# Optimization experiments

Measured on AMD Instinct MI355X. Metric: run time of the kernel, lower is better.

The kernel has to match this reference:

```python
import jax, jax.numpy as jnp
import numpy as np

B, S, H, L = 64, 512, 768, 21


def setup_inputs() -> dict:
    key = jax.random.key(0)
    ks = jax.random.split(key, 8)
    hidden = jax.random.normal(ks[0], (B, S, H), dtype=jnp.float32)
    attention_mask = jnp.ones((B, S), dtype=jnp.int32)
    labels = jax.random.randint(ks[1], (B, S), 0, L, dtype=jnp.int64)
    W = jax.random.normal(ks[2], (H, L), dtype=jnp.float32) * 0.02
    b = jnp.zeros((L,), dtype=jnp.float32)
    start_transitions = jax.random.uniform(ks[3], (L,), minval=-0.1, maxval=0.1)
    end_transitions = jax.random.uniform(ks[4], (L,), minval=-0.1, maxval=0.1)
    transitions = jax.random.uniform(ks[5], (L, L), minval=-0.1, maxval=0.1)
    return {"hidden": hidden, "attention_mask": attention_mask, "labels": labels,
            "W": W, "b": b, "start_transitions": start_transitions,
            "end_transitions": end_transitions, "transitions": transitions}


def _crf_llh(emissions, tags, mask, start, end, trans):
    # torchcrf log-likelihood, batch_first. emissions [B,S,L], tags [B,S], mask [B,S] bool
    maskf = mask.astype(emissions.dtype)
    first_tags = tags[:, 0]
    num = start[first_tags] + jnp.take_along_axis(emissions[:, 0], first_tags[:, None], axis=1)[:, 0]
    trans_scores = trans[tags[:, :-1], tags[:, 1:]]                         # [B,S-1]
    emit_scores = jnp.take_along_axis(emissions, tags[:, :, None], axis=2)[:, :, 0]  # [B,S]
    num = num + jnp.sum((trans_scores + emit_scores[:, 1:]) * maskf[:, 1:], axis=1)
    seq_ends = jnp.sum(mask.astype(jnp.int32), axis=1) - 1
    last_tags = jnp.take_along_axis(tags, seq_ends[:, None], axis=1)[:, 0]
    num = num + end[last_tags]
    # denominator: forward algorithm as a scan over time
    def step(score, xs):
        emit_t, m_t = xs  # [B,L], [B]
        nxt = jax.nn.logsumexp(score[:, :, None] + trans[None] + emit_t[:, None, :], axis=1)
        return jnp.where(m_t[:, None], nxt, score), None
    score0 = start[None] + emissions[:, 0]
    xs = (jnp.transpose(emissions[:, 1:], (1, 0, 2)), mask[:, 1:].T)
    scoreT, _ = jax.lax.scan(step, score0, xs)
    denom = jax.nn.logsumexp(scoreT + end[None], axis=1)
    return num - denom


def _viterbi_one_hot(emissions, mask, start, end, trans):
    # Viterbi decode (max-plus scan) + backtrack, returns one-hot logits like _decoded_to_one_hot
    def fstep(score, xs):
        emit_t, m_t = xs
        cand = score[:, :, None] + trans[None]     # [B,L,L]
        idx = jnp.argmax(cand, axis=1)             # [B,L] best previous tag
        nxt = jnp.max(cand, axis=1) + emit_t
        return jnp.where(m_t[:, None], nxt, score), idx
    score0 = start[None] + emissions[:, 0]
    xs = (jnp.transpose(emissions[:, 1:], (1, 0, 2)), mask[:, 1:].T)
    scoreT, hist = jax.lax.scan(fstep, score0, xs)   # hist [S-1,B,L]
    best_last = jnp.argmax(scoreT + end[None], axis=1)  # [B]
    def bstep(carry, xs):
        h_t, m_t = xs
        prev = jnp.take_along_axis(h_t, carry[:, None], axis=1)[:, 0]
        return jnp.where(m_t, prev, carry), carry
    tag0, tags_rest = jax.lax.scan(bstep, best_last, (hist, mask[:, 1:].T), reverse=True)
    tags = jnp.concatenate([tag0[:, None], tags_rest.T], axis=1)  # [B,S]
    one_hot = jax.nn.one_hot(tags, emissions.shape[-1], dtype=emissions.dtype)
    return one_hot * mask[:, :, None].astype(emissions.dtype)


def reference(hidden, attention_mask, labels, W, b, start_transitions, end_transitions, transitions):
    mask = attention_mask.astype(bool)
    emissions = jnp.einsum('bsh,hl->bsl', hidden, W) + b  # classifier (dropout = identity in eval)
    logits = _viterbi_one_hot(emissions, mask, start_transitions, end_transitions, transitions)
    # loss path: replicate forward's tag/mask fixups
    tags = jnp.where(labels < 0, 0, labels).at[:, 0].set(0)
    valid = (mask & (labels >= 0)).at[:, 0].set(True)
    llh = _crf_llh(emissions, tags, valid, start_transitions, end_transitions, transitions)
    loss = -jnp.mean(llh)
    return loss, logits
```

## Files before the change

kernel.cpp:

```cpp
#include <hip/hip_runtime.h>
#include <math.h>

#define BB 64
#define SS 512
#define HH 768
#define LL 21
#define STR 513
#define INFF __builtin_huge_valf()

__device__ inline float rlf(float v, int i) {
    return __int_as_float(__builtin_amdgcn_readlane(__float_as_int(v), i));
}
__device__ inline float mx3(float a, float b, float c) { return fmaxf(fmaxf(a, b), c); }
__device__ inline float wmax64(float v) {
    #pragma unroll
    for (int off = 32; off; off >>= 1) v = fmaxf(v, __shfl_xor(v, off));
    return v;
}
__device__ inline float rlmax21(float a) {
    float r0 = mx3(rlf(a, 0), rlf(a, 1), rlf(a, 2));
    float r1 = mx3(rlf(a, 3), rlf(a, 4), rlf(a, 5));
    float r2 = mx3(rlf(a, 6), rlf(a, 7), rlf(a, 8));
    float r3 = mx3(rlf(a, 9), rlf(a, 10), rlf(a, 11));
    float r4 = mx3(rlf(a, 12), rlf(a, 13), rlf(a, 14));
    float r5 = mx3(rlf(a, 15), rlf(a, 16), rlf(a, 17));
    float r6 = mx3(rlf(a, 18), rlf(a, 19), rlf(a, 20));
    return mx3(mx3(r0, r1, r2), mx3(r3, r4, r5), r6);
}

__global__ __launch_bounds__(128) void k_emis(const float* __restrict__ hidden,
                                              const float* __restrict__ W,
                                              const float* __restrict__ bias,
                                              float* __restrict__ em0,
                                              float* __restrict__ em1,
                                              float* __restrict__ em2,
                                              float* __restrict__ em3) {
    __shared__ float Wl[192 * 24];
    int tid = threadIdx.x;
    int q = blockIdx.x & 3;
    int rg = blockIdx.x >> 2;
    int row = rg * 128 + tid;
    const float* hp = hidden + (size_t)row * HH + q * 192;
    const float4* Wq4 = reinterpret_cast<const float4*>(W + q * 192 * LL);

    for (int f = tid; f < 1008; f += 128) {
        float4 v = Wq4[f];
        int e0 = 4 * f;
        { int e = e0,     k = e / 21, l = e - 21 * k; Wl[k * 24 + l] = v.x; }
        { int e = e0 + 1, k = e / 21, l = e - 21 * k; Wl[k * 24 + l] = v.y; }
        { int e = e0 + 2, k = e / 21, l = e - 21 * k; Wl[k * 24 + l] = v.z; }
        { int e = e0 + 3, k = e / 21, l = e - 21 * k; Wl[k * 24 + l] = v.w; }
    }
    __syncthreads();

    float acc[LL];
    #pragma unroll
    for (int l = 0; l < LL; ++l) acc[l] = 0.f;

#define FMAK(HV, WB) do { \
    float hv_ = (HV); \
    float4 q0 = *reinterpret_cast<const float4*>(WB); \
    float4 q1 = *reinterpret_cast<const float4*>((WB) + 4); \
    float4 q2 = *reinterpret_cast<const float4*>((WB) + 8); \
    float4 q3 = *reinterpret_cast<const float4*>((WB) + 12); \
    float4 q4 = *reinterpret_cast<const float4*>((WB) + 16); \
    float q20 = (WB)[20]; \
    acc[0]  = fmaf(hv_, q0.x, acc[0]);  acc[1]  = fmaf(hv_, q0.y, acc[1]); \
    acc[2]  = fmaf(hv_, q0.z, acc[2]);  acc[3]  = fmaf(hv_, q0.w, acc[3]); \
    acc[4]  = fmaf(hv_, q1.x, acc[4]);  acc[5]  = fmaf(hv_, q1.y, acc[5]); \
    acc[6]  = fmaf(hv_, q1.z, acc[6]);  acc[7]  = fmaf(hv_, q1.w, acc[7]); \
    acc[8]  = fmaf(hv_, q2.x, acc[8]);  acc[9]  = fmaf(hv_, q2.y, acc[9]); \
    acc[10] = fmaf(hv_, q2.z, acc[10]); acc[11] = fmaf(hv_, q2.w, acc[11]); \
    acc[12] = fmaf(hv_, q3.x, acc[12]); acc[13] = fmaf(hv_, q3.y, acc[13]); \
    acc[14] = fmaf(hv_, q3.z, acc[14]); acc[15] = fmaf(hv_, q3.w, acc[15]); \
    acc[16] = fmaf(hv_, q4.x, acc[16]); acc[17] = fmaf(hv_, q4.y, acc[17]); \
    acc[18] = fmaf(hv_, q4.z, acc[18]); acc[19] = fmaf(hv_, q4.w, acc[19]); \
    acc[20] = fmaf(hv_, q20, acc[20]); } while (0)

    float4 ha = *reinterpret_cast<const float4*>(hp);
    for (int c = 0; c < 48; ++c) {
        float4 hn = ha;
        if (c + 1 < 48) hn = *reinterpret_cast<const float4*>(hp + (c + 1) * 4);
        const float* wb = Wl + (c * 4) * 24;
        FMAK(ha.x, wb);
        FMAK(ha.y, wb + 24);
        FMAK(ha.z, wb + 48);
        FMAK(ha.w, wb + 72);
        ha = hn;
    }
#undef FMAK

    float* emr = (q == 0 ? em0 : q == 1 ? em1 : q == 2 ? em2 : em3) + (size_t)row * LL;
    if (q == 0) {
        #pragma unroll
        for (int l = 0; l < LL; ++l) emr[l] = acc[l] + bias[l];
    } else {
        #pragma unroll
        for (int l = 0; l < LL; ++l) emr[l] = acc[l];
    }
}

__global__ __launch_bounds__(64) void k_scan(const float* __restrict__ em0,
                                             const float* __restrict__ em1,
                                             const float* __restrict__ em2,
                                             const float* __restrict__ em3,
                                             const int* __restrict__ attn,
                                             const int* __restrict__ labels,
                                             const float* __restrict__ startT,
                                             const float* __restrict__ endT,
                                             const float* __restrict__ trans,
                                             float* __restrict__ num,
                                             float* __restrict__ denom,
                                             float* __restrict__ Sout) {
    __shared__ float eLT[LL * STR + 8];
    int lane = threadIdx.x;
    int bid = blockIdx.x;
    bool act = lane < LL;
    int jj = act ? lane : (LL - 1);

    if (bid < 128) {
        int b = bid & 63;
        size_t boff = (size_t)b * SS * LL;
        const float* emb0 = em0 + boff;
        const float* emb1 = em1 + boff;
        const float* emb2 = em2 + boff;
        const float* emb3 = em3 + boff;
        const int* mrow = attn + b * SS;

        for (int f = lane; f < (SS * LL) / 4; f += 64) {
            float4 v0 = *reinterpret_cast<const float4*>(emb0 + 4 * f);
            float4 v1 = *reinterpret_cast<const float4*>(emb1 + 4 * f);
            float4 v2 = *reinterpret_cast<const float4*>(emb2 + 4 * f);
            float4 v3 = *reinterpret_cast<const float4*>(emb3 + 4 * f);
            float4 v = make_float4((v0.x + v1.x) + (v2.x + v3.x),
                                   (v0.y + v1.y) + (v2.y + v3.y),
                                   (v0.z + v1.z) + (v2.z + v3.z),
                                   (v0.w + v1.w) + (v2.w + v3.w));
            unsigned e0 = 4u * (unsigned)f;
            { unsigned t = e0 / 21u,       j = e0 - 21u * t;       eLT[j * STR + t] = v.x; }
            { unsigned e = e0 + 1, t = e / 21u, j = e - 21u * t;   eLT[j * STR + t] = v.y; }
            { unsigned e = e0 + 2, t = e / 21u, j = e - 21u * t;   eLT[j * STR + t] = v.z; }
            { unsigned e = e0 + 3, t = e / 21u, j = e - 21u * t;   eLT[j * STR + t] = v.w; }
        }
        __syncthreads();

        int jbase = jj * STR;
        float A0, A1, A2, A3, B0, B1, B2, B3;

#define LDG(P, G) do { int t4_ = (G) * 4; \
    P##0 = eLT[jbase + t4_];     P##1 = eLT[jbase + t4_ + 1]; \
    P##2 = eLT[jbase + t4_ + 2]; P##3 = eLT[jbase + t4_ + 3]; } while (0)

        if (bid < 64) {
            float Tc[LL];
            #pragma unroll
            for (int i = 0; i < LL; ++i) Tc[i] = trans[i * LL + jj];
            float* Sgj = Sout + (size_t)b * (LL * SS) + jj * SS;

#define VCORE(EMIT, BIT) do { \
    float sv_[LL]; \
    _Pragma("unroll") for (int i_ = 0; i_ < LL; ++i_) sv_[i_] = rlf(a, i_); \
    __builtin_amdgcn_sched_barrier(0); \
    float cd_[LL]; \
    _Pragma("unroll") for (int i_ = 0; i_ < LL; ++i_) cd_[i_] = sv_[i_] + Tc[i_]; \
    float x0 = mx3(cd_[0], cd_[1], cd_[2]),   x1 = mx3(cd_[3], cd_[4], cd_[5]); \
    float x2 = mx3(cd_[6], cd_[7], cd_[8]),   x3 = mx3(cd_[9], cd_[10], cd_[11]); \
    float x4 = mx3(cd_[12], cd_[13], cd_[14]), x5 = mx3(cd_[15], cd_[16], cd_[17]); \
    float x6 = mx3(cd_[18], cd_[19], cd_[20]); \
    float best = mx3(mx3(x0, x1, x2), mx3(x3, x4, x5), x6); \
    bool mt_ = ((mm >> (BIT)) & 1ull) != 0ull; \
    float an_ = best + (EMIT); \
    a = (mt_ && act) ? an_ : a; \
} while (0)
#define VGROUPR(P, TB, BB0) do { \
    float o0_, o1_, o2_, o3_; \
    VCORE(P##0, (BB0));     o0_ = a; \
    VCORE(P##1, (BB0) + 1); o1_ = a; \
    VCORE(P##2, (BB0) + 2); o2_ = a; \
    VCORE(P##3, (BB0) + 3); o3_ = a; \
    if (act) *reinterpret_cast<float4*>(Sgj + (TB)) = make_float4(o0_, o1_, o2_, o3_); \
} while (0)

            LDG(A, 0); LDG(B, 1);
            int mk0 = mrow[lane];
            unsigned long long mm = __ballot(mk0 != 0);
            mk0 = mrow[64 + lane];
            float a = act ? (startT[lane] + A0) : -INFF;
            {
                float o0_ = a, o1_, o2_, o3_;
                VCORE(A1, 1); o1_ = a;
                VCORE(A2, 2); o2_ = a;
                VCORE(A3, 3); o3_ = a;
                if (act) *reinterpret_cast<float4*>(Sgj) = make_float4(o0_, o1_, o2_, o3_);
                LDG(A, 2);
                VGROUPR(B, 4, 4);
                LDG(B, 3);
            }
            for (int gg = 1; gg < 64; ++gg) {
                if ((gg & 7) == 0) {
                    mm = __ballot(mk0 != 0);
                    if (gg != 56) mk0 = mrow[((gg >> 3) + 1) * 64 + lane];
                }
                int bb = (gg & 7) * 8;
                VGROUPR(A, 8 * gg, bb);
                LDG(A, 2 * gg + 2);
                VGROUPR(B, 8 * gg + 4, bb + 4);
                LDG(B, 2 * gg + 3);
            }
#undef VCORE
#undef VGROUPR
        } else {
            float Ec[LL];
            #pragma unroll
            for (int i = 0; i < LL; ++i) Ec[i] = __expf(trans[i * LL + jj]);

#define LCORE(EMIT, BIT) do { \
    float x_ = __expf(a - M); \
    float sv_[LL]; \
    _Pragma("unroll") for (int i_ = 0; i_ < LL; ++i_) sv_[i_] = rlf(x_, i_); \
    __builtin_amdgcn_sched_barrier(0); \
    float g0_ = sv_[0] * Ec[0]; \
    _Pragma("unroll") for (int i_ = 1; i_ < 7; ++i_)  g0_ = fmaf(sv_[i_], Ec[i_], g0_); \
    float g1_ = sv_[7] * Ec[7]; \
    _Pragma("unroll") for (int i_ = 8; i_ < 14; ++i_) g1_ = fmaf(sv_[i_], Ec[i_], g1_); \
    float g2_ = sv_[14] * Ec[14]; \
    _Pragma("unroll") for (int i_ = 15; i_ < 21; ++i_) g2_ = fmaf(sv_[i_], Ec[i_], g2_); \
    float Ss_ = (g0_ + g1_) + g2_; \
    bool mt_ = ((mm >> (BIT)) & 1ull) != 0ull; \
    float an_ = M + __logf(Ss_) + (EMIT); \
    a = (mt_ && act) ? an_ : a; \
} while (0)

            LDG(A, 0); LDG(B, 1);
            int mk0 = mrow[lane];
            unsigned long long mm = __ballot(mk0 != 0);
            mk0 = mrow[64 + lane];
            float a = act ? (startT[lane] + A0) : -INFF;
            float M = rlmax21(a);
            {
                LCORE(A1, 1); LCORE(A2, 2); LCORE(A3, 3);
                LDG(A, 2);
                LCORE(B0, 4); LCORE(B1, 5); LCORE(B2, 6); LCORE(B3, 7);
                LDG(B, 3);
            }
            for (int gg = 1; gg < 64; ++gg) {
                if ((gg & 7) == 0) {
                    mm = __ballot(mk0 != 0);
                    if (gg != 56) mk0 = mrow[((gg >> 3) + 1) * 64 + lane];
                }
                M = rlmax21(a);
                int bb = (gg & 7) * 8;
                LCORE(A0, bb);     LCORE(A1, bb + 1); LCORE(A2, bb + 2); LCORE(A3, bb + 3);
                LDG(A, 2 * gg + 2);
                LCORE(B0, bb + 4); LCORE(B1, bb + 5); LCORE(B2, bb + 6); LCORE(B3, bb + 7);
                LDG(B, 2 * gg + 3);
            }
#undef LCORE
            float f = act ? (a + endT[lane]) : -INFF;
            float m = wmax64(f);
            float p = act ? __expf(f - m) : 0.f;
            #pragma unroll
            for (int off = 32; off; off >>= 1) p += __shfl_xor(p, off);
            if (lane == 0) denom[b] = m + __logf(p);
        }
#undef LDG
    } else {
        int b = bid - 128;
        const int* lrow = labels + b * SS;
        const int* arow = attn + b * SS;
        float psum = 0.f;
        int pcnt = 0;
        for (int s = 0; s < 8; ++s) {
            int t = s * 64 + lane;
            int lab = lrow[t];
            int mk = arow[t];
            int valid = (t == 0) ? 1 : ((mk != 0 && lab >= 0) ? 1 : 0);
            if (t >= 1 && valid) {
                int tag = (lab < 0) ? 0 : lab;
                int labp = lrow[t - 1];
                int tagp = (t == 1) ? 0 : ((labp < 0) ? 0 : labp);
                size_t ei = ((size_t)b * SS + t) * LL + tag;
                psum += trans[tagp * LL + tag] + ((em0[ei] + em1[ei]) + (em2[ei] + em3[ei]));
            }
            pcnt += valid;
        }
        #pragma unroll
        for (int off = 32; off; off >>= 1) {
            psum += __shfl_xor(psum, off);
            pcnt += __shfl_xor(pcnt, off);
        }
        int ts = pcnt - 1;
        int labL = lrow[ts];
        int tagL = (ts == 0) ? 0 : ((labL < 0) ? 0 : labL);
        if (lane == 0) {
            size_t e0i = (size_t)b * SS * LL;
            num[b] = startT[0] + ((em0[e0i] + em1[e0i]) + (em2[e0i] + em3[e0i]))
                   + psum + endT[tagL];
        }
    }
}

__global__ __launch_bounds__(512) void k_back(const float* __restrict__ S,
                                              const int* __restrict__ attn,
                                              const float* __restrict__ endT,
                                              const float* __restrict__ trans,
                                              const float* __restrict__ num,
                                              const float* __restrict__ denom,
                                              float* __restrict__ out) {
    __shared__ float Sl[LL][517];
    __shared__ unsigned char pred[SS * 24];
    __shared__ unsigned char mapL[64 * 32];
    __shared__ float Tl[441];
    __shared__ int tg_s[SS];
    int tid = threadIdx.x, b = blockIdx.x;
    const float* SB = S + (size_t)b * (LL * SS);
    for (int i = tid; i < 441; i += 512) Tl[i] = trans[i];
    for (int f = tid; f < (LL * SS) / 4; f += 512) {
        float4 v = *reinterpret_cast<const float4*>(SB + 4 * f);
        int j = f >> 7, t0 = (f & 127) * 4;
        Sl[j][t0] = v.x; Sl[j][t0 + 1] = v.y; Sl[j][t0 + 2] = v.z; Sl[j][t0 + 3] = v.w;
    }
    if (b == 0 && tid < 64) {
        float llh = num[tid] - denom[tid];
        #pragma unroll
        for (int off = 32; off; off >>= 1) llh += __shfl_xor(llh, off);
        if (tid == 0) out[0] = -llh / (float)BB;
    }
    __syncthreads();

    for (int u = tid; u < 511 * LL; u += 512) {
        int t = 1 + u / LL;
        int j = u - (u / LL) * LL;
        unsigned int pj = (unsigned int)j;
        if (attn[b * SS + t] != 0) {
            float bv = Sl[0][t - 1] + Tl[j];
            unsigned int bi = 0;
            #pragma unroll
            for (int i = 1; i < LL; ++i) {
                float c = Sl[i][t - 1] + Tl[i * LL + j];
                bool g = c > bv;
                bv = g ? c : bv;
                bi = g ? (unsigned int)i : bi;
            }
            pj = bi;
        }
        pred[t * 24 + j] = (unsigned char)pj;
    }
    __syncthreads();

    if (tid < 64) {
        int lane = tid;
        float f = (lane < LL) ? (Sl[lane][SS - 1] + endT[lane]) : -INFF;
        float m = wmax64(f);
        unsigned long long msk = __ballot(f == m);
        int best_last = __ffsll(msk) - 1;

        int tlo = 8 * lane + 1;
        int thi = 8 * lane + 8; if (thi > 511) thi = 511;
        unsigned int BM[LL];
        #pragma unroll
        for (int s = 0; s < LL; ++s) BM[s] = s;
        for (int k = 0; k < 8; ++k) {
            int t = thi - k;
            if (t >= tlo) {
                #pragma unroll
                for (int s = 0; s < LL; ++s) BM[s] = pred[t * 24 + BM[s]];
            }
        }
        #pragma unroll
        for (int s = 0; s < LL; ++s) mapL[lane * 32 + s] = (unsigned char)BM[s];

        #pragma unroll
        for (int kk = 1; kk < 64; kk <<= 1) {
            int p = lane + kk;
            bool vld = p < 64;
            int pp = vld ? p : 0;
            unsigned int P[LL];
            #pragma unroll
            for (int s = 0; s < LL; ++s) {
                unsigned int v = mapL[pp * 32 + s];
                P[s] = vld ? v : (unsigned int)s;
            }
            unsigned int N[LL];
            #pragma unroll
            for (int s = 0; s < LL; ++s) N[s] = mapL[lane * 32 + P[s]];
            #pragma unroll
            for (int s = 0; s < LL; ++s) mapL[lane * 32 + s] = (unsigned char)N[s];
        }

        int st8 = mapL[lane * 32 + best_last];
        int nxt = __shfl(st8, lane + 1);
        int cur = (lane == 63) ? best_last : nxt;
        for (int k = 0; k < 8; ++k) {
            int t = thi - k;
            if (t >= tlo) {
                tg_s[t] = cur;
                cur = pred[t * 24 + cur];
            }
        }
        if (lane == 0) tg_s[0] = cur;
    }
    __syncthreads();

    {
        int t = tid;
        int tag = tg_s[t];
        int mk = attn[b * SS + t];
        float* o = out + 1 + ((size_t)b * SS + t) * LL;
        #pragma unroll
        for (int l = 0; l < LL; ++l) o[l] = (mk && tag == l) ? 1.f : 0.f;
    }
}

extern "C" void kernel_launch(void* const* d_in, const int* in_sizes, int n_in,
                              void* d_out, int out_size, void* d_ws, size_t ws_size,
                              hipStream_t stream) {
    const float* hidden = (const float*)d_in[0];
    const int*   attn   = (const int*)d_in[1];
    const int*   labels = (const int*)d_in[2];
    const float* W      = (const float*)d_in[3];
    const float* bias   = (const float*)d_in[4];
    const float* startT = (const float*)d_in[5];
    const float* endT   = (const float*)d_in[6];
    const float* trans  = (const float*)d_in[7];
    float* out = (float*)d_out;

    float* wsf   = (float*)d_ws;
    size_t emsz  = (size_t)BB * SS * LL;
    float* em0   = wsf;
    float* em1   = em0 + emsz;
    float* em2   = em1 + emsz;
    float* em3   = em2 + emsz;
    float* num   = em3 + emsz;
    float* denom = num + 64;
    float* Sbuf  = out + 4;

    hipLaunchKernelGGL(k_emis, dim3(1024), dim3(128), 0, stream, hidden, W, bias,
                       em0, em1, em2, em3);
    hipLaunchKernelGGL(k_scan, dim3(192), dim3(64),  0, stream, em0, em1, em2, em3,
                       attn, labels, startT, endT, trans, num, denom, Sbuf);
    hipLaunchKernelGGL(k_back, dim3(64),  dim3(512), 0, stream, Sbuf, attn, endT, trans,
                       num, denom, out);
}
```

Before: 146.5 us.

## Split 21-way recurrence reduction across three lane groups via ds_bpermute

The Viterbi and forward-algorithm recurrences no longer have each lane read all 21 previous scores with 21 readlanes. Lanes are now split into three groups of 21 (lanes 0-62), each covering 7 source states through ds_bpermute. Partial results are then combined with two more bpermutes. This cuts per-step scalar readlane serialization and per-lane ALU work, but adds LDS-crossbar permute latency on the serial dependency chain. The code assumes lanes 0-20 keep their state mapping and that the result is valid there.

```diff
diff --git a/kernel.cpp b/kernel.cpp
--- a/kernel.cpp
+++ b/kernel.cpp
@@ -10,6 +10,9 @@
 
 __device__ inline float rlf(float v, int i) {
     return __int_as_float(__builtin_amdgcn_readlane(__float_as_int(v), i));
+}
+__device__ inline float bpf(int i4, float v) {
+    return __int_as_float(__builtin_amdgcn_ds_bpermute(i4, __float_as_int(v)));
 }
 __device__ inline float mx3(float a, float b, float c) { return fmaxf(fmaxf(a, b), c); }
 __device__ inline float wmax64(float v) {
@@ -144,6 +147,14 @@
         }
         __syncthreads();
 
+        int st = lane % LL;
+        int g  = lane / LL; if (g > 2) g = 2;
+        int ix[7];
+        #pragma unroll
+        for (int i2 = 0; i2 < 7; ++i2) ix[i2] = (7 * g + i2) * 4;
+        int cx1 = (st + LL) * 4;
+        int cx2 = (st + 2 * LL) * 4;
+
         int jbase = jj * STR;
         float A0, A1, A2, A3, B0, B1, B2, B3;
 
@@ -152,22 +163,21 @@
     P##2 = eLT[jbase + t4_ + 2]; P##3 = eLT[jbase + t4_ + 3]; } while (0)
 
         if (bid < 64) {
-            float Tc[LL];
-            #pragma unroll
-            for (int i = 0; i < LL; ++i) Tc[i] = trans[i * LL + jj];
+            float Tg[7];
+            #pragma unroll
+            for (int i2 = 0; i2 < 7; ++i2) Tg[i2] = trans[(7 * g + i2) * LL + st];
             float* Sgj = Sout + (size_t)b * (LL * SS) + jj * SS;
 
 #define VCORE(EMIT, BIT) do { \
-    float sv_[LL]; \
-    _Pragma("unroll") for (int i_ = 0; i_ < LL; ++i_) sv_[i_] = rlf(a, i_); \
-    __builtin_amdgcn_sched_barrier(0); \
-    float cd_[LL]; \
-    _Pragma("unroll") for (int i_ = 0; i_ < LL; ++i_) cd_[i_] = sv_[i_] + Tc[i_]; \
-    float x0 = mx3(cd_[0], cd_[1], cd_[2]),   x1 = mx3(cd_[3], cd_[4], cd_[5]); \
-    float x2 = mx3(cd_[6], cd_[7], cd_[8]),   x3 = mx3(cd_[9], cd_[10], cd_[11]); \
-    float x4 = mx3(cd_[12], cd_[13], cd_[14]), x5 = mx3(cd_[15], cd_[16], cd_[17]); \
-    float x6 = mx3(cd_[18], cd_[19], cd_[20]); \
-    float best = mx3(mx3(x0, x1, x2), mx3(x3, x4, x5), x6); \
+    float s0_ = bpf(ix[0], a), s1_ = bpf(ix[1], a), s2_ = bpf(ix[2], a); \
+    float s3_ = bpf(ix[3], a), s4_ = bpf(ix[4], a), s5_ = bpf(ix[5], a); \
+    float s6_ = bpf(ix[6], a); \
+    float c0_ = s0_ + Tg[0], c1_ = s1_ + Tg[1], c2_ = s2_ + Tg[2]; \
+    float c3_ = s3_ + Tg[3], c4_ = s4_ + Tg[4], c5_ = s5_ + Tg[5]; \
+    float c6_ = s6_ + Tg[6]; \
+    float pb_ = mx3(mx3(c0_, c1_, c2_), mx3(c3_, c4_, c5_), c6_); \
+    float q1_ = bpf(cx1, pb_), q2_ = bpf(cx2, pb_); \
+    float best = mx3(pb_, q1_, q2_); \
     bool mt_ = ((mm >> (BIT)) & 1ull) != 0ull; \
     float an_ = best + (EMIT); \
     a = (mt_ && act) ? an_ : a; \
@@ -210,22 +220,21 @@
 #undef VCORE
 #undef VGROUPR
         } else {
-            float Ec[LL];
-            #pragma unroll
-            for (int i = 0; i < LL; ++i) Ec[i] = __expf(trans[i * LL + jj]);
+            float Eg[7];
+            #pragma unroll
+            for (int i2 = 0; i2 < 7; ++i2) Eg[i2] = __expf(trans[(7 * g + i2) * LL + st]);
 
 #define LCORE(EMIT, BIT) do { \
     float x_ = __expf(a - M); \
-    float sv_[LL]; \
-    _Pragma("unroll") for (int i_ = 0; i_ < LL; ++i_) sv_[i_] = rlf(x_, i_); \
-    __builtin_amdgcn_sched_barrier(0); \
-    float g0_ = sv_[0] * Ec[0]; \
-    _Pragma("unroll") for (int i_ = 1; i_ < 7; ++i_)  g0_ = fmaf(sv_[i_], Ec[i_], g0_); \
-    float g1_ = sv_[7] * Ec[7]; \
-    _Pragma("unroll") for (int i_ = 8; i_ < 14; ++i_) g1_ = fmaf(sv_[i_], Ec[i_], g1_); \
-    float g2_ = sv_[14] * Ec[14]; \
-    _Pragma("unroll") for (int i_ = 15; i_ < 21; ++i_) g2_ = fmaf(sv_[i_], Ec[i_], g2_); \
-    float Ss_ = (g0_ + g1_) + g2_; \
+    float s0_ = bpf(ix[0], x_), s1_ = bpf(ix[1], x_), s2_ = bpf(ix[2], x_); \
+    float s3_ = bpf(ix[3], x_), s4_ = bpf(ix[4], x_), s5_ = bpf(ix[5], x_); \
+    float s6_ = bpf(ix[6], x_); \
+    float ps_ = s0_ * Eg[0]; \
+    ps_ = fmaf(s1_, Eg[1], ps_); ps_ = fmaf(s2_, Eg[2], ps_); \
+    ps_ = fmaf(s3_, Eg[3], ps_); ps_ = fmaf(s4_, Eg[4], ps_); \
+    ps_ = fmaf(s5_, Eg[5], ps_); ps_ = fmaf(s6_, Eg[6], ps_); \
+    float q1_ = bpf(cx1, ps_), q2_ = bpf(cx2, ps_); \
+    float Ss_ = (ps_ + q1_) + q2_; \
     bool mt_ = ((mm >> (BIT)) & 1ull) != 0ull; \
     float an_ = M + __logf(Ss_) + (EMIT); \
     a = (mt_ && act) ? an_ : a; \
```

Result: slower. 155.2 us (+5.9%).
